# Kernel optimization log

Measured on AMD Instinct MI355X. Metric: run time of the kernel, lower is better.

The kernel has to match this reference:

```python
import jax, jax.numpy as jnp
import numpy as np

COMPLEXES = 2048
RESX = 16
RESY = 16
RATE = 16
FEAT = 64


def setup_inputs() -> dict:
    key = jax.random.key(0)
    k1, k2, k3 = jax.random.split(key, 3)
    P = RATE * RATE  # samples per complex
    map_ = jax.random.normal(k1, (COMPLEXES, RESY, RESX, FEAT), dtype=jnp.float32)
    u = jax.random.uniform(k2, (COMPLEXES, P), dtype=jnp.float32)
    v = jax.random.uniform(k3, (COMPLEXES, P), dtype=jnp.float32)
    return {"map": map_, "u": u, "v": v}


def reference(map, u, v):
    # map: [complexes, resy, resx, feat]; u, v: [complexes, P] in [0,1]
    C, H, W, F = map.shape
    x = u * (W - 1)
    y = v * (H - 1)
    x0 = jnp.clip(jnp.floor(x).astype(jnp.int32), 0, W - 2)
    y0 = jnp.clip(jnp.floor(y).astype(jnp.int32), 0, H - 2)
    fx = (x - x0.astype(x.dtype))[..., None]  # [C, P, 1]
    fy = (y - y0.astype(y.dtype))[..., None]
    cidx = jnp.arange(C)[:, None]  # [C, 1] broadcast over samples
    g00 = map[cidx, y0, x0]          # [C, P, F]
    g01 = map[cidx, y0, x0 + 1]
    g10 = map[cidx, y0 + 1, x0]
    g11 = map[cidx, y0 + 1, x0 + 1]
    top = g00 * (1.0 - fx) + g01 * fx
    bot = g10 * (1.0 - fx) + g11 * fx
    return top * (1.0 - fy) + bot * fy  # [C, P, F]
```

## Files before the change

kernel.cpp:

```cpp
#include <hip/hip_runtime.h>

constexpr int C_ = 2048;
constexpr int H_ = 16;
constexpr int W_ = 16;
constexpr int F_ = 64;
constexpr int P_ = 256;
constexpr int MAP4 = H_ * W_ * F_ / 4;

__global__ __launch_bounds__(256) void ngf_fetch_kernel(
    const float* __restrict__ map_,
    const float* __restrict__ u_,
    const float* __restrict__ v_,
    float* __restrict__ out_) {
  __shared__ float4 smap[MAP4];
  __shared__ float s_fx[P_];
  __shared__ float s_fy[P_];
  __shared__ int   s_ix[P_];

  const int c = blockIdx.x;
  const int tid = threadIdx.x;

  const float4* gmap = (const float4*)(map_ + (size_t)c * (H_ * W_ * F_));
#pragma unroll
  for (int i = 0; i < MAP4 / 256; ++i) {
    smap[i * 256 + tid] = gmap[i * 256 + tid];
  }

  {
    const float x = u_[(size_t)c * P_ + tid] * (float)(W_ - 1);
    const float y = v_[(size_t)c * P_ + tid] * (float)(H_ - 1);
    int x0 = (int)floorf(x);
    int y0 = (int)floorf(y);
    x0 = x0 < 0 ? 0 : (x0 > W_ - 2 ? W_ - 2 : x0);
    y0 = y0 < 0 ? 0 : (y0 > H_ - 2 ? H_ - 2 : y0);
    s_fx[tid] = x - (float)x0;
    s_fy[tid] = y - (float)y0;
    s_ix[tid] = (y0 * W_ + x0) * (F_ / 4);
  }
  __syncthreads();

  float4* gout = (float4*)(out_ + (size_t)c * (P_ * F_));
  const int f = tid & 15;
  const int sbase = tid >> 4;

#pragma unroll
  for (int it = 0; it < 16; ++it) {
    const int s = it * 16 + sbase;
    const float fx = s_fx[s];
    const float fy = s_fy[s];
    const int ix = s_ix[s] + f;

    const float4 g00 = smap[ix];
    const float4 g01 = smap[ix + (F_ / 4)];
    const float4 g10 = smap[ix + W_ * (F_ / 4)];
    const float4 g11 = smap[ix + (W_ + 1) * (F_ / 4)];

    const float wx1 = fx, wx0 = 1.0f - fx;
    const float wy1 = fy, wy0 = 1.0f - fy;

    float4 r;
    r.x = (g00.x * wx0 + g01.x * wx1) * wy0 + (g10.x * wx0 + g11.x * wx1) * wy1;
    r.y = (g00.y * wx0 + g01.y * wx1) * wy0 + (g10.y * wx0 + g11.y * wx1) * wy1;
    r.z = (g00.z * wx0 + g01.z * wx1) * wy0 + (g10.z * wx0 + g11.z * wx1) * wy1;
    r.w = (g00.w * wx0 + g01.w * wx1) * wy0 + (g10.w * wx0 + g11.w * wx1) * wy1;

    gout[s * (F_ / 4) + f] = r;
  }
}

extern "C" void kernel_launch(void* const* d_in, const int* in_sizes, int n_in,
                              void* d_out, int out_size, void* d_ws, size_t ws_size,
                              hipStream_t stream) {
  const float* map_ = (const float*)d_in[0];
  const float* u_   = (const float*)d_in[1];
  const float* v_   = (const float*)d_in[2];
  float* out_ = (float*)d_out;

  ngf_fetch_kernel<<<C_, 256, 0, stream>>>(map_, u_, v_, out_);
}
```

Baseline: 237.8 us.

## Replace LDS map staging with direct L2-cached gathers and XCD-aware block mapping

Drops the per-complex shared-memory copy of the 64 KB feature map. Each block now handles 16 samples and gathers the four bilinear corners straight from global memory. Block indices are remapped so all 16 blocks of one complex land on the same XCD, so their repeated gathers should hit that XCD's L2. The launch grows to 32768 small blocks with no LDS or barrier, which raises occupancy; the cost is relying on cache hits for roughly four-fold redundant reads. Clamping also changes from floor to truncation, which is only valid because inputs are nonnegative.

```diff
diff --git a/kernel.cpp b/kernel.cpp
--- a/kernel.cpp
+++ b/kernel.cpp
@@ -5,67 +5,46 @@
 constexpr int W_ = 16;
 constexpr int F_ = 64;
 constexpr int P_ = 256;
-constexpr int MAP4 = H_ * W_ * F_ / 4;
 
-__global__ __launch_bounds__(256) void ngf_fetch_kernel(
+__global__ __launch_bounds__(256) void ngf_gather_kernel(
     const float* __restrict__ map_,
     const float* __restrict__ u_,
     const float* __restrict__ v_,
     float* __restrict__ out_) {
-  __shared__ float4 smap[MAP4];
-  __shared__ float s_fx[P_];
-  __shared__ float s_fy[P_];
-  __shared__ int   s_ix[P_];
+  const int g   = blockIdx.x;
+  const int xcd = g & 7;
+  const int q   = g >> 3;
+  const int c   = (xcd << 8) | (q >> 4);
+  const int sub = q & 15;
 
-  const int c = blockIdx.x;
   const int tid = threadIdx.x;
+  const int f   = tid & 15;
+  const int s   = (sub << 4) | (tid >> 4);
 
-  const float4* gmap = (const float4*)(map_ + (size_t)c * (H_ * W_ * F_));
-#pragma unroll
-  for (int i = 0; i < MAP4 / 256; ++i) {
-    smap[i * 256 + tid] = gmap[i * 256 + tid];
-  }
+  const float x = u_[c * P_ + s] * (float)(W_ - 1);
+  const float y = v_[c * P_ + s] * (float)(H_ - 1);
+  int x0 = (int)x; x0 = x0 > W_ - 2 ? W_ - 2 : x0;
+  int y0 = (int)y; y0 = y0 > H_ - 2 ? H_ - 2 : y0;
+  const float fx = x - (float)x0;
+  const float fy = y - (float)y0;
 
-  {
-    const float x = u_[(size_t)c * P_ + tid] * (float)(W_ - 1);
-    const float y = v_[(size_t)c * P_ + tid] * (float)(H_ - 1);
-    int x0 = (int)floorf(x);
-    int y0 = (int)floorf(y);
-    x0 = x0 < 0 ? 0 : (x0 > W_ - 2 ? W_ - 2 : x0);
-    y0 = y0 < 0 ? 0 : (y0 > H_ - 2 ? H_ - 2 : y0);
-    s_fx[tid] = x - (float)x0;
-    s_fy[tid] = y - (float)y0;
-    s_ix[tid] = (y0 * W_ + x0) * (F_ / 4);
-  }
-  __syncthreads();
+  const float4* base = (const float4*)map_ + (((size_t)c) << 12)
+                     + (y0 * W_ + x0) * (F_ / 4) + f;
+  const float4 g00 = base[0];
+  const float4 g01 = base[F_ / 4];
+  const float4 g10 = base[W_ * (F_ / 4)];
+  const float4 g11 = base[(W_ + 1) * (F_ / 4)];
 
-  float4* gout = (float4*)(out_ + (size_t)c * (P_ * F_));
-  const int f = tid & 15;
-  const int sbase = tid >> 4;
+  const float wx1 = fx, wx0 = 1.0f - fx;
+  const float wy1 = fy, wy0 = 1.0f - fy;
 
-#pragma unroll
-  for (int it = 0; it < 16; ++it) {
-    const int s = it * 16 + sbase;
-    const float fx = s_fx[s];
-    const float fy = s_fy[s];
-    const int ix = s_ix[s] + f;
+  float4 r;
+  r.x = (g00.x * wx0 + g01.x * wx1) * wy0 + (g10.x * wx0 + g11.x * wx1) * wy1;
+  r.y = (g00.y * wx0 + g01.y * wx1) * wy0 + (g10.y * wx0 + g11.y * wx1) * wy1;
+  r.z = (g00.z * wx0 + g01.z * wx1) * wy0 + (g10.z * wx0 + g11.z * wx1) * wy1;
+  r.w = (g00.w * wx0 + g01.w * wx1) * wy0 + (g10.w * wx0 + g11.w * wx1) * wy1;
 
-    const float4 g00 = smap[ix];
-    const float4 g01 = smap[ix + (F_ / 4)];
-    const float4 g10 = smap[ix + W_ * (F_ / 4)];
-    const float4 g11 = smap[ix + (W_ + 1) * (F_ / 4)];
-
-    const float wx1 = fx, wx0 = 1.0f - fx;
-    const float wy1 = fy, wy0 = 1.0f - fy;
-
-    float4 r;
-    r.x = (g00.x * wx0 + g01.x * wx1) * wy0 + (g10.x * wx0 + g11.x * wx1) * wy1;
-    r.y = (g00.y * wx0 + g01.y * wx1) * wy0 + (g10.y * wx0 + g11.y * wx1) * wy1;
-    r.z = (g00.z * wx0 + g01.z * wx1) * wy0 + (g10.z * wx0 + g11.z * wx1) * wy1;
-    r.w = (g00.w * wx0 + g01.w * wx1) * wy0 + (g10.w * wx0 + g11.w * wx1) * wy1;
-
-    gout[s * (F_ / 4) + f] = r;
-  }
+  ((float4*)out_)[(((size_t)c) << 12) + s * (F_ / 4) + f] = r;
 }
 
 extern "C" void kernel_launch(void* const* d_in, const int* in_sizes, int n_in,
@@ -76,5 +55,6 @@
   const float* v_   = (const float*)d_in[2];
   float* out_ = (float*)d_out;
 
-  ngf_fetch_kernel<<<C_, 256, 0, stream>>>(map_, u_, v_, out_);
+  const int blocks = C_ * (P_ / 16);
+  ngf_gather_kernel<<<blocks, 256, 0, stream>>>(map_, u_, v_, out_);
 }
```

Result: slower. 251.0 us (+5.5%).
